# Kernel tuning notes

Measured on AMD Instinct MI355X. Metric: run time of the kernel, lower is better.

The kernel has to match this reference:

```python
import jax, jax.numpy as jnp
import numpy as np
from functools import partial

FS = 30.0
CUTOFF = 3.3
ORDER = 5
PADLEN = 18  # scipy filtfilt default: 3 * max(len(a), len(b)) = 3 * 6


def butter_lowpass_np(order, Wn):
    """Digital Butterworth lowpass (b, a), matching scipy.signal.butter."""
    # analog prototype poles (buttap)
    m = np.arange(-order + 1, order, 2)
    p = -np.exp(1j * np.pi * m / (2 * order))
    k = 1.0
    # pre-warp frequency (scipy uses internal fs = 2.0)
    fs = 2.0
    warped = 2 * fs * np.tan(np.pi * Wn / fs)
    p = warped * p
    k = k * warped ** order
    # bilinear transform
    fs2 = 2 * fs
    p_z = (fs2 + p) / (fs2 - p)
    z_z = -np.ones(order)
    k_z = k * np.real(1.0 / np.prod(fs2 - p))
    b = k_z * np.real(np.poly(z_z))
    a = np.real(np.poly(p_z))
    return b.astype(np.float64), a.astype(np.float64)


def lfilter_zi_np(b, a):
    """Steady-state initial conditions, matching scipy.signal.lfilter_zi."""
    n = len(a)
    comp = np.zeros((n - 1, n - 1))
    comp[0, :] = -a[1:] / a[0]
    if n > 2:
        comp[1:, :-1] = np.eye(n - 2)
    B = b[1:] - a[1:] * b[0]
    return np.linalg.solve(np.eye(n - 1) - comp.T, B)


def lfilter(b, a, x, zi):
    """Direct-form II transposed IIR filter along a 1-D signal via lax.scan."""
    def step(z, xt):
        y = b[0] * xt + z[0]
        z_shift = jnp.concatenate([z[1:], jnp.zeros(1, z.dtype)])
        z_new = b[1:] * xt + z_shift - a[1:] * y
        return z_new, y
    _, y = jax.lax.scan(step, zi, x)
    return y


def filtfilt_1d(b, a, zi, x):
    """Zero-phase filtering with odd-extension padding (scipy filtfilt defaults)."""
    left = 2 * x[0] - x[PADLEN:0:-1]
    right = 2 * x[-1] - x[-2:-(PADLEN + 2):-1]
    ext = jnp.concatenate([left, x, right])
    y = lfilter(b, a, ext, zi * ext[0])
    y = lfilter(b, a, y[::-1], zi * y[-1])[::-1]
    return y[PADLEN:-PADLEN]


def setup_inputs() -> dict:
    key = jax.random.key(0)
    x = jax.random.normal(key, (4096, 8192), dtype=jnp.float32)
    Wn = CUTOFF / (FS / 2.0)
    b_np, a_np = butter_lowpass_np(ORDER, Wn)
    zi_np = lfilter_zi_np(b_np, a_np)
    return {
        "x": x,
        "b": jnp.asarray(b_np, dtype=jnp.float32),
        "a": jnp.asarray(a_np, dtype=jnp.float32),
        "zi": jnp.asarray(zi_np, dtype=jnp.float32),
    }


def reference(x, b, a, zi):
    # batched zero-phase Butterworth lowpass, [batch, length] -> [batch, length]
    return jax.vmap(partial(filtfilt_1d, b, a, zi))(x)
```

## Files before the change

kernel.cpp:

```cpp
#include <hip/hip_runtime.h>


#define NN   8192
#define PADL 18
#define LC   64
#define TPB  128

__device__ __forceinline__ float4 LDQ(const float* b, int c, int j) {
    return *reinterpret_cast<const float4*>(b + (c << 6) + ((j ^ (c & 15)) << 2));
}
__device__ __forceinline__ void STQ(float* b, int c, int j, float4 v) {
    *reinterpret_cast<float4*>(b + (c << 6) + ((j ^ (c & 15)) << 2)) = v;
}
__device__ __forceinline__ float SC(const float* b, int c, int e) {
    return b[(c << 6) + (((e >> 2) ^ (c & 15)) << 2) + (e & 3)];
}

#define STEP(xv) do {                               \
    float y_ = fmaf(b0, (xv), z0);                  \
    z0 = fmaf(na1, y_, fmaf(b1, (xv), z1));         \
    z1 = fmaf(na2, y_, fmaf(b2, (xv), z2));         \
    z2 = fmaf(na3, y_, fmaf(b3, (xv), z3));         \
    z3 = fmaf(na4, y_, fmaf(b4, (xv), z4));         \
    z4 = fmaf(na5, y_, b5 * (xv));                  \
    yv = y_;                                        \
} while (0)

__global__ __launch_bounds__(TPB, 2) void GREEN_62869731278967_filtfilt(
    const float* __restrict__ x,
    const float* __restrict__ bc,
    const float* __restrict__ ac,
    const float* __restrict__ zc,
    float* __restrict__ out)
{
    __shared__ float B[NN];
    const int tid = threadIdx.x;
    const float* xr   = x   + (size_t)blockIdx.x * NN;
    float*       outr = out + (size_t)blockIdx.x * NN;

    const float b0 = bc[0], b1 = bc[1], b2 = bc[2], b3 = bc[3], b4 = bc[4], b5 = bc[5];
    const float na1 = -ac[1], na2 = -ac[2], na3 = -ac[3], na4 = -ac[4], na5 = -ac[5];
    const float zi0 = zc[0], zi1 = zc[1], zi2 = zc[2], zi3 = zc[3], zi4 = zc[4];

#pragma unroll
    for (int q = 0; q < 16; ++q) {
        float4 v = *reinterpret_cast<const float4*>(xr + (q << 9) + (tid << 2));
        STQ(B, (q << 3) + (tid >> 4), tid & 15, v);
    }
    __syncthreads();

    float yreg[LC];
    float ytail[PADL];
    float z0, z1, z2, z3, z4, yv;

    if (tid == 0) {
        const float x0 = B[0];
        float v0 = 2.f * x0 - B[PADL];
        z0 = zi0 * v0; z1 = zi1 * v0; z2 = zi2 * v0; z3 = zi3 * v0; z4 = zi4 * v0;
#pragma unroll
        for (int t = 0; t < PADL; ++t) {
            float v = 2.f * x0 - B[PADL - t];
            STEP(v);
        }
    } else {
        const int cp = tid - 1;
        float4 q8 = LDQ(B, cp, 8);
        z0 = zi0 * q8.x; z1 = zi1 * q8.x; z2 = zi2 * q8.x; z3 = zi3 * q8.x; z4 = zi4 * q8.x;
        STEP(q8.x); STEP(q8.y); STEP(q8.z); STEP(q8.w);
#pragma unroll
        for (int j = 9; j < 16; ++j) {
            float4 q = LDQ(B, cp, j);
            STEP(q.x); STEP(q.y); STEP(q.z); STEP(q.w);
        }
    }
#pragma unroll
    for (int j = 0; j < 16; ++j) {
        float4 q = LDQ(B, tid, j);
        STEP(q.x); yreg[4 * j + 0] = yv;
        STEP(q.y); yreg[4 * j + 1] = yv;
        STEP(q.z); yreg[4 * j + 2] = yv;
        STEP(q.w); yreg[4 * j + 3] = yv;
    }
    if (tid == TPB - 1) {
        const float xN = SC(B, TPB - 1, 63);
#pragma unroll
        for (int i = 0; i < PADL; ++i) {
            float v = 2.f * xN - SC(B, TPB - 1, 62 - i);
            STEP(v);
            ytail[i] = yv;
        }
    }
    __syncthreads();

#pragma unroll
    for (int j = 0; j < 8; ++j)
        STQ(B, tid, j, make_float4(yreg[4 * j], yreg[4 * j + 1],
                                   yreg[4 * j + 2], yreg[4 * j + 3]));
    __syncthreads();

    if (tid == TPB - 1) {
        float u0 = ytail[PADL - 1];
        z0 = zi0 * u0; z1 = zi1 * u0; z2 = zi2 * u0; z3 = zi3 * u0; z4 = zi4 * u0;
#pragma unroll
        for (int s = 0; s < PADL; ++s) STEP(ytail[PADL - 1 - s]);
    } else {
        const int cn = tid + 1;
        float4 q7 = LDQ(B, cn, 7);
        z0 = zi0 * q7.w; z1 = zi1 * q7.w; z2 = zi2 * q7.w; z3 = zi3 * q7.w; z4 = zi4 * q7.w;
        STEP(q7.w); STEP(q7.z); STEP(q7.y); STEP(q7.x);
#pragma unroll
        for (int j = 6; j >= 0; --j) {
            float4 q = LDQ(B, cn, j);
            STEP(q.w); STEP(q.z); STEP(q.y); STEP(q.x);
        }
    }
#pragma unroll
    for (int j = 15; j >= 0; --j) {
        STEP(yreg[4 * j + 3]); yreg[4 * j + 3] = yv;
        STEP(yreg[4 * j + 2]); yreg[4 * j + 2] = yv;
        STEP(yreg[4 * j + 1]); yreg[4 * j + 1] = yv;
        STEP(yreg[4 * j + 0]); yreg[4 * j + 0] = yv;
    }

#pragma unroll
    for (int k = 0; k < 16; ++k) {
        float4 v;
        v.x = yreg[4 * k + 0];
        v.y = yreg[4 * k + 1];
        v.z = yreg[4 * k + 2];
        v.w = yreg[4 * k + 3];
        *reinterpret_cast<float4*>(outr + (tid << 6) + (k << 2)) = v;
    }
}

extern "C" void kernel_launch(void* const* d_in, const int* in_sizes, int n_in,
                              void* d_out, int out_size, void* d_ws, size_t ws_size,
                              hipStream_t stream) {
    const float* x  = (const float*)d_in[0];
    const float* b  = (const float*)d_in[1];
    const float* a  = (const float*)d_in[2];
    const float* zi = (const float*)d_in[3];
    float* out = (float*)d_out;
    const int rows = in_sizes[0] / NN;
    GREEN_62869731278967_filtfilt<<<rows, TPB, 0, stream>>>(x, b, a, zi, out);
}
```

Baseline: 72.99 us.

## Split each row into four single-wavefront segments with halo windows

Each row is now handled by four blocks of one 64-thread wavefront, each covering a 2048-sample segment. The shared window carries a 32-sample halo on either side, so neighbouring chunks warm up the filter state without touching other blocks. Because a block is a single wavefront, the __syncthreads calls become LDS waitcnt plus sched barriers, and per-thread register arrays shrink from 64 to 32 floats, which should allow more resident waves. The cost is loading the halos twice, and the last lane now runs serial warm-up steps for the neighbouring segment.

Result: slower. 77.57 us (+6.3%).

```diff
diff --git a/kernel.cpp b/kernel.cpp
--- a/kernel.cpp
+++ b/kernel.cpp
@@ -2,19 +2,24 @@
 
 
 #define NN   8192
+#define SEG  2048
+#define NSEG 4
 #define PADL 18
-#define LC   64
-#define TPB  128
+#define TPB  64
+#define WIN  2112
 
 __device__ __forceinline__ float4 LDQ(const float* b, int c, int j) {
-    return *reinterpret_cast<const float4*>(b + (c << 6) + ((j ^ (c & 15)) << 2));
+    return *reinterpret_cast<const float4*>(b + (c << 5) + ((j ^ (c & 7)) << 2));
 }
 __device__ __forceinline__ void STQ(float* b, int c, int j, float4 v) {
-    *reinterpret_cast<float4*>(b + (c << 6) + ((j ^ (c & 15)) << 2)) = v;
+    *reinterpret_cast<float4*>(b + (c << 5) + ((j ^ (c & 7)) << 2)) = v;
 }
 __device__ __forceinline__ float SC(const float* b, int c, int e) {
-    return b[(c << 6) + (((e >> 2) ^ (c & 15)) << 2) + (e & 3)];
+    return b[(c << 5) + (((e >> 2) ^ (c & 7)) << 2) + (e & 3)];
 }
+
+#define WAITL() do { asm volatile("s_waitcnt lgkmcnt(0)" ::: "memory");   \
+                     __builtin_amdgcn_sched_barrier(0); } while (0)
 
 #define STEP(xv) do {                               \
     float y_ = fmaf(b0, (xv), z0);                  \
@@ -26,110 +31,148 @@
     yv = y_;                                        \
 } while (0)
 
-__global__ __launch_bounds__(TPB, 2) void GREEN_62869731278967_filtfilt(
+__global__ __launch_bounds__(TPB, 4) void GREEN_62869731278967_filtfilt(
     const float* __restrict__ x,
     const float* __restrict__ bc,
     const float* __restrict__ ac,
     const float* __restrict__ zc,
     float* __restrict__ out)
 {
-    __shared__ float B[NN];
-    const int tid = threadIdx.x;
-    const float* xr   = x   + (size_t)blockIdx.x * NN;
-    float*       outr = out + (size_t)blockIdx.x * NN;
+    __shared__ float B[WIN];
+    const int l    = threadIdx.x;
+    const int row  = blockIdx.x >> 2;
+    const int segi = blockIdx.x & 3;
+    const int seg  = segi << 11;
+    const bool first = (segi == 0);
+    const bool last  = (segi == NSEG - 1);
+    const float* xrow = x   + (size_t)row * NN;
+    float*       orow = out + (size_t)row * NN;
 
     const float b0 = bc[0], b1 = bc[1], b2 = bc[2], b3 = bc[3], b4 = bc[4], b5 = bc[5];
     const float na1 = -ac[1], na2 = -ac[2], na3 = -ac[3], na4 = -ac[4], na5 = -ac[5];
     const float zi0 = zc[0], zi1 = zc[1], zi2 = zc[2], zi3 = zc[3], zi4 = zc[4];
 
+    {
+        const int base = seg - 32;
 #pragma unroll
-    for (int q = 0; q < 16; ++q) {
-        float4 v = *reinterpret_cast<const float4*>(xr + (q << 9) + (tid << 2));
-        STQ(B, (q << 3) + (tid >> 4), tid & 15, v);
+        for (int k = 0; k < 8; ++k) {
+            int g  = (k << 6) + l;
+            int s4 = base + (g << 2);
+            s4 = s4 < 0 ? 0 : (s4 > NN - 4 ? NN - 4 : s4);
+            float4 v = *reinterpret_cast<const float4*>(xrow + s4);
+            STQ(B, g >> 3, g & 7, v);
+        }
+        if (l < 16) {
+            int g  = 512 + l;
+            int s4 = base + (g << 2);
+            s4 = s4 < 0 ? 0 : (s4 > NN - 4 ? NN - 4 : s4);
+            float4 v = *reinterpret_cast<const float4*>(xrow + s4);
+            STQ(B, g >> 3, g & 7, v);
+        }
     }
-    __syncthreads();
+    WAITL();
 
-    float yreg[LC];
-    float ytail[PADL];
+    float yreg[32];
+    float ynx[32];
     float z0, z1, z2, z3, z4, yv;
 
-    if (tid == 0) {
-        const float x0 = B[0];
-        float v0 = 2.f * x0 - B[PADL];
+    if (first && l == 0) {
+        const float x0 = SC(B, 1, 0);
+        float v0 = 2.f * x0 - SC(B, 1, PADL);
         z0 = zi0 * v0; z1 = zi1 * v0; z2 = zi2 * v0; z3 = zi3 * v0; z4 = zi4 * v0;
 #pragma unroll
         for (int t = 0; t < PADL; ++t) {
-            float v = 2.f * x0 - B[PADL - t];
+            float v = 2.f * x0 - SC(B, 1, PADL - t);
             STEP(v);
         }
     } else {
-        const int cp = tid - 1;
-        float4 q8 = LDQ(B, cp, 8);
-        z0 = zi0 * q8.x; z1 = zi1 * q8.x; z2 = zi2 * q8.x; z3 = zi3 * q8.x; z4 = zi4 * q8.x;
-        STEP(q8.x); STEP(q8.y); STEP(q8.z); STEP(q8.w);
+        float4 q0 = LDQ(B, l, 0);
+        z0 = zi0 * q0.x; z1 = zi1 * q0.x; z2 = zi2 * q0.x; z3 = zi3 * q0.x; z4 = zi4 * q0.x;
+        STEP(q0.x); STEP(q0.y); STEP(q0.z); STEP(q0.w);
 #pragma unroll
-        for (int j = 9; j < 16; ++j) {
-            float4 q = LDQ(B, cp, j);
+        for (int j = 1; j < 8; ++j) {
+            float4 q = LDQ(B, l, j);
             STEP(q.x); STEP(q.y); STEP(q.z); STEP(q.w);
         }
     }
 #pragma unroll
-    for (int j = 0; j < 16; ++j) {
-        float4 q = LDQ(B, tid, j);
+    for (int j = 0; j < 8; ++j) {
+        float4 q = LDQ(B, l + 1, j);
         STEP(q.x); yreg[4 * j + 0] = yv;
         STEP(q.y); yreg[4 * j + 1] = yv;
         STEP(q.z); yreg[4 * j + 2] = yv;
         STEP(q.w); yreg[4 * j + 3] = yv;
     }
-    if (tid == TPB - 1) {
-        const float xN = SC(B, TPB - 1, 63);
+    if (l == TPB - 1) {
+        if (last) {
+            const float xN = SC(B, 64, 31);
 #pragma unroll
-        for (int i = 0; i < PADL; ++i) {
-            float v = 2.f * xN - SC(B, TPB - 1, 62 - i);
-            STEP(v);
-            ytail[i] = yv;
+            for (int i = 0; i < PADL; ++i) {
+                float v = 2.f * xN - SC(B, 64, 30 - i);
+                STEP(v);
+                ynx[i] = yv;
+            }
+        } else {
+#pragma unroll
+            for (int j = 0; j < 8; ++j) {
+                float4 q = LDQ(B, 65, j);
+                STEP(q.x); ynx[4 * j + 0] = yv;
+                STEP(q.y); ynx[4 * j + 1] = yv;
+                STEP(q.z); ynx[4 * j + 2] = yv;
+                STEP(q.w); ynx[4 * j + 3] = yv;
+            }
         }
     }
-    __syncthreads();
 
+    __builtin_amdgcn_sched_barrier(0);
 #pragma unroll
     for (int j = 0; j < 8; ++j)
-        STQ(B, tid, j, make_float4(yreg[4 * j], yreg[4 * j + 1],
-                                   yreg[4 * j + 2], yreg[4 * j + 3]));
-    __syncthreads();
+        STQ(B, l + 1, j, make_float4(yreg[4 * j], yreg[4 * j + 1],
+                                     yreg[4 * j + 2], yreg[4 * j + 3]));
+    WAITL();
 
-    if (tid == TPB - 1) {
-        float u0 = ytail[PADL - 1];
-        z0 = zi0 * u0; z1 = zi1 * u0; z2 = zi2 * u0; z3 = zi3 * u0; z4 = zi4 * u0;
+    if (l == TPB - 1) {
+        if (last) {
+            float u0 = ynx[PADL - 1];
+            z0 = zi0 * u0; z1 = zi1 * u0; z2 = zi2 * u0; z3 = zi3 * u0; z4 = zi4 * u0;
 #pragma unroll
-        for (int s = 0; s < PADL; ++s) STEP(ytail[PADL - 1 - s]);
+            for (int s = 0; s < PADL; ++s) STEP(ynx[PADL - 1 - s]);
+        } else {
+            float u0 = ynx[31];
+            z0 = zi0 * u0; z1 = zi1 * u0; z2 = zi2 * u0; z3 = zi3 * u0; z4 = zi4 * u0;
+#pragma unroll
+            for (int j = 7; j >= 0; --j) {
+                STEP(ynx[4 * j + 3]); STEP(ynx[4 * j + 2]);
+                STEP(ynx[4 * j + 1]); STEP(ynx[4 * j + 0]);
+            }
+        }
     } else {
-        const int cn = tid + 1;
-        float4 q7 = LDQ(B, cn, 7);
+        float4 q7 = LDQ(B, l + 2, 7);
         z0 = zi0 * q7.w; z1 = zi1 * q7.w; z2 = zi2 * q7.w; z3 = zi3 * q7.w; z4 = zi4 * q7.w;
         STEP(q7.w); STEP(q7.z); STEP(q7.y); STEP(q7.x);
 #pragma unroll
         for (int j = 6; j >= 0; --j) {
-            float4 q = LDQ(B, cn, j);
+            float4 q = LDQ(B, l + 2, j);
             STEP(q.w); STEP(q.z); STEP(q.y); STEP(q.x);
         }
     }
 #pragma unroll
-    for (int j = 15; j >= 0; --j) {
+    for (int j = 7; j >= 0; --j) {
         STEP(yreg[4 * j + 3]); yreg[4 * j + 3] = yv;
         STEP(yreg[4 * j + 2]); yreg[4 * j + 2] = yv;
         STEP(yreg[4 * j + 1]); yreg[4 * j + 1] = yv;
         STEP(yreg[4 * j + 0]); yreg[4 * j + 0] = yv;
     }
 
+    float* od = orow + seg + (l << 5);
 #pragma unroll
-    for (int k = 0; k < 16; ++k) {
+    for (int k = 0; k < 8; ++k) {
         float4 v;
         v.x = yreg[4 * k + 0];
         v.y = yreg[4 * k + 1];
         v.z = yreg[4 * k + 2];
         v.w = yreg[4 * k + 3];
-        *reinterpret_cast<float4*>(outr + (tid << 6) + (k << 2)) = v;
+        *reinterpret_cast<float4*>(od + (k << 2)) = v;
     }
 }
 
@@ -142,5 +185,5 @@
     const float* zi = (const float*)d_in[3];
     float* out = (float*)d_out;
     const int rows = in_sizes[0] / NN;
-    GREEN_62869731278967_filtfilt<<<rows, TPB, 0, stream>>>(x, b, a, zi, out);
+    GREEN_62869731278967_filtfilt<<<rows * NSEG, TPB, 0, stream>>>(x, b, a, zi, out);
 }
```
